# Kernel optimization log

Measured on AMD Instinct MI355X. Metric: run time of the kernel, lower is better.

## Reference

```python
import jax, jax.numpy as jnp
import numpy as np


def setup_inputs() -> dict:
    key = jax.random.key(0)
    ks = jax.random.split(key, 8)
    B, S, F, K, E, N = 20000, 10, 128, 16, 128, 200000
    nodes = jax.random.randint(ks[0], (B,), 0, N)
    neigh_idx = jax.random.randint(ks[1], (B, S), 0, N)
    self_table = jax.random.normal(ks[2], (N, F), dtype=jnp.float32)
    neigh_table = jax.random.normal(ks[3], (N, F), dtype=jnp.float32)
    center = jax.random.normal(ks[4], (K, F), dtype=jnp.float32)
    cluster_mask = jax.random.uniform(ks[5], (K, F), dtype=jnp.float32)
    # xavier-like scaling keeps exp(relu(.)) in a sane range
    weight = jax.random.normal(ks[6], (E, 2 * F), dtype=jnp.float32) * 0.05
    alpha = jax.random.normal(ks[7], (2 * F, 1), dtype=jnp.float32) * 0.05
    return {"nodes": nodes, "neigh_idx": neigh_idx, "self_table": self_table,
            "neigh_table": neigh_table, "center": center, "cluster_mask": cluster_mask,
            "weight": weight, "alpha": alpha}


def reference(nodes, neigh_idx, self_table, neigh_table, center, cluster_mask, weight, alpha):
    B, S = neigh_idx.shape
    F = self_table.shape[1]
    self_feat = self_table[nodes]                       # (B, F)
    neigh = neigh_table[neigh_idx]                      # (B, S, F) gather (== mask.matmul in original)
    # attention over sampled neighbors: exp(relu([self || neigh] @ alpha))
    a_self, a_neigh = alpha[:F, 0], alpha[F:, 0]        # split cat-matmul
    logits = self_feat @ a_self                         # (B,)
    logits = logits[:, None] + neigh @ a_neigh          # (B, S)
    att = jnp.exp(jax.nn.relu(logits))
    att_norm = att / jnp.sum(att, axis=1, keepdims=True)
    # inverse-distance soft assignment to k centers (Student-t, degree 1)
    n2 = jnp.sum(neigh * neigh, axis=-1)                # (B, S)
    c2 = jnp.sum(center * center, axis=-1)              # (K,)
    cross = jnp.einsum('bsf,kf->bsk', neigh, center)    # (B, S, K)
    q = 1.0 / (n2[:, :, None] - 2.0 * cross + c2[None, None, :] + 1.0)  # (B, S, K)
    # clustered features: sum_k q[b,s,k] * mask[k,f] * neigh[b,s,f]
    clustered = neigh * jnp.einsum('bsk,kf->bsf', q, cluster_mask)      # (B, S, F)
    neigh_agg = jnp.sum(clustered * att_norm[:, :, None], axis=1)       # (B, F)
    combined = jnp.concatenate([self_feat, neigh_agg], axis=1)          # (B, 2F)
    return jax.nn.relu(combined @ weight.T)                             # (B, E)
```

## Files before the change

kernel.cpp:

```cpp
#include <hip/hip_runtime.h>
#include <hip/hip_bf16.h>

typedef unsigned short ushort_t;
typedef __attribute__((ext_vector_type(4))) float v4f;
typedef __attribute__((ext_vector_type(8))) short v8s;

#define FDIM 128
#define KCLUST 16
#define CSTRIDE 264
#define QSTRIDE 24
#define SS 10

__device__ __forceinline__ ushort_t f2bf(float x) {
    unsigned int u = __float_as_uint(x);
    unsigned int r = (u + 0x7fffu + ((u >> 16) & 1u)) >> 16;
    return (ushort_t)r;
}
__device__ __forceinline__ float bf2f(ushort_t h) {
    return __uint_as_float((unsigned int)h << 16);
}
__device__ __forceinline__ float wave_reduce_sum(float v) {
    #pragma unroll
    for (int off = 32; off > 0; off >>= 1) v += __shfl_xor(v, off, 64);
    return v;
}

union V8U { v8s v; ushort_t u[8]; };

__global__ void pack_weight(const float* __restrict__ W, ushort_t* __restrict__ Wb,
                            long total, long valid) {
    long i = ((long)blockIdx.x * blockDim.x + threadIdx.x) * 4;
    if (i >= total) return;
    float4 v;
    if (i < valid) v = *(const float4*)(W + i);
    else           v = make_float4(0.f, 0.f, 0.f, 0.f);
    ushort_t* dst = Wb + i;
    dst[0] = f2bf(v.x); dst[1] = f2bf(v.y); dst[2] = f2bf(v.z); dst[3] = f2bf(v.w);
}

__global__ __launch_bounds__(512, 2) void fused_agg_s10(
    const int* __restrict__ nodes, const int* __restrict__ neigh_idx,
    const float* __restrict__ self_table, const float* __restrict__ neigh_table,
    const float* __restrict__ center, const float* __restrict__ cluster_mask,
    const float* __restrict__ alpha, const ushort_t* __restrict__ Wb,
    float* __restrict__ out, int B, int E) {

    __shared__ __align__(16) ushort_t comb[16 * CSTRIDE];
    __shared__ __align__(16) ushort_t nbf[SS * 16 * 128];
    __shared__ __align__(16) ushort_t qhi[SS * 16 * QSTRIDE];
    __shared__ __align__(16) ushort_t qlo[SS * 16 * QSTRIDE];
    __shared__ __align__(16) float    attL[SS * 16];
    __shared__ __align__(16) float    n2L[SS * 16];
    __shared__ __align__(16) int      idxL[SS * 16];

    const int t    = threadIdx.x;
    const int lane = t & 63, wave = t >> 6;
    const int g    = t >> 5;
    const int fq   = t & 31;
    const int f0   = fq << 2;
    const int l16  = lane & 15, quad = lane >> 4;

    const int b0 = blockIdx.x * 16;
    int bg = b0 + g; if (bg >= B) bg = B - 1;

    const float4 aS = *(const float4*)(alpha + f0);
    const float4 aN = *(const float4*)(alpha + FDIM + f0);

    float ls;
    {
        size_t node = (size_t)nodes[bg];
        float4 sf = *(const float4*)(self_table + node * FDIM + f0);
        ushort_t h0 = f2bf(sf.x), h1 = f2bf(sf.y), h2 = f2bf(sf.z), h3 = f2bf(sf.w);
        uint2 pk;
        pk.x = (unsigned)h0 | ((unsigned)h1 << 16);
        pk.y = (unsigned)h2 | ((unsigned)h3 << 16);
        *(uint2*)(comb + g * CSTRIDE + f0) = pk;
        ls = sf.x * aS.x + sf.y * aS.y + sf.z * aS.z + sf.w * aS.w;
        #pragma unroll
        for (int off = 1; off <= 16; off <<= 1) ls += __shfl_xor(ls, off, 64);
    }

    v8s cbf[4]; float c2v = 0.f;
    {
        const float* crow = center + l16 * FDIM;
        #pragma unroll
        for (int kk = 0; kk < 4; kk++) {
            const float* p = crow + kk * 32 + quad * 8;
            float4 x = *(const float4*)p;
            float4 y = *(const float4*)(p + 4);
            V8U pk;
            pk.u[0] = f2bf(x.x); pk.u[1] = f2bf(x.y); pk.u[2] = f2bf(x.z); pk.u[3] = f2bf(x.w);
            pk.u[4] = f2bf(y.x); pk.u[5] = f2bf(y.y); pk.u[6] = f2bf(y.z); pk.u[7] = f2bf(y.w);
            cbf[kk] = pk.v;
            c2v += x.x*x.x + x.y*x.y + x.z*x.z + x.w*x.w
                 + y.x*y.x + y.y*y.y + y.z*y.z + y.w*y.w;
        }
        c2v += __shfl_xor(c2v, 16, 64);
        c2v += __shfl_xor(c2v, 32, 64);
    }

    v8s mhi, mlo;
    {
        V8U ph, pl;
        const int fc = wave * 16 + l16;
        #pragma unroll
        for (int j = 0; j < 8; j++) {
            float mv = (quad < 2) ? cluster_mask[(quad * 8 + j) * FDIM + fc] : 0.f;
            ushort_t h = f2bf(mv);
            ph.u[j] = h; pl.u[j] = f2bf(mv - bf2f(h));
        }
        mhi = ph.v; mlo = pl.v;
    }

    int idxv[SS];
    #pragma unroll
    for (int j = 0; j < SS; j++) idxv[j] = neigh_idx[(size_t)bg * SS + j];
    if (fq == 0) {
        #pragma unroll
        for (int j = 0; j < SS; j++) idxL[j * 16 + g] = idxv[j];
    }

    #pragma unroll
    for (int j = 0; j < SS; j++) {
        const float4 cur = *(const float4*)(neigh_table + (size_t)idxv[j] * FDIM + f0);
        {
            ushort_t h0 = f2bf(cur.x), h1 = f2bf(cur.y), h2 = f2bf(cur.z), h3 = f2bf(cur.w);
            uint2 pk;
            pk.x = (unsigned)h0 | ((unsigned)h1 << 16);
            pk.y = (unsigned)h2 | ((unsigned)h3 << 16);
            const int slot = (fq >> 1) ^ g;
            *(uint2*)((char*)nbf + (j * 16 + g) * 256 + slot * 16 + (fq & 1) * 8) = pk;
        }
        float pn = cur.x * aN.x + cur.y * aN.y + cur.z * aN.z + cur.w * aN.w;
        float p2 = cur.x * cur.x + cur.y * cur.y + cur.z * cur.z + cur.w * cur.w;
        #pragma unroll
        for (int off = 1; off <= 16; off <<= 1) {
            pn += __shfl_xor(pn, off, 64);
            p2 += __shfl_xor(p2, off, 64);
        }
        const float att = __expf(fmaxf(ls + pn, 0.f));
        if (fq == 0) { attL[j * 16 + g] = att; n2L[j * 16 + g] = p2; }
    }

    asm volatile("s_waitcnt lgkmcnt(0)" ::: "memory");
    __builtin_amdgcn_s_barrier();
    asm volatile("" ::: "memory");

    const int fcol = wave * 16 + l16;
    float nReg[SS * 4];
    #pragma unroll
    for (int s = 0; s < SS; s++) {
        const int4 iv = *(const int4*)&idxL[s * 16 + quad * 4];
        nReg[s * 4 + 0] = neigh_table[(size_t)iv.x * FDIM + fcol];
        nReg[s * 4 + 1] = neigh_table[(size_t)iv.y * FDIM + fcol];
        nReg[s * 4 + 2] = neigh_table[(size_t)iv.z * FDIM + fcol];
        nReg[s * 4 + 3] = neigh_table[(size_t)iv.w * FDIM + fcol];
    }

    for (int s = wave; s < SS; s += 8) {
        v4f xacc = {0.f, 0.f, 0.f, 0.f};
        #pragma unroll
        for (int kk = 0; kk < 4; kk++) {
            const int sl = (kk * 4 + quad) ^ l16;
            v8s af = *(const v8s*)((const char*)nbf + (s * 16 + l16) * 256 + sl * 16);
            xacc = __builtin_amdgcn_mfma_f32_16x16x32_bf16(af, cbf[kk], xacc, 0, 0, 0);
        }
        const float4 n2r = *(const float4*)&n2L[s * 16 + quad * 4];
        #pragma unroll
        for (int r = 0; r < 4; r++) {
            const float n2v = (r == 0) ? n2r.x : (r == 1) ? n2r.y : (r == 2) ? n2r.z : n2r.w;
            const float d  = n2v - 2.f * xacc[r] + c2v;
            const float qv = 1.f / (d + 1.f);
            const ushort_t h = f2bf(qv);
            qhi[(s * 16 + quad * 4 + r) * QSTRIDE + l16] = h;
            qlo[(s * 16 + quad * 4 + r) * QSTRIDE + l16] = f2bf(qv - bf2f(h));
        }
    }

    asm volatile("s_waitcnt lgkmcnt(0)" ::: "memory");
    __builtin_amdgcn_s_barrier();
    asm volatile("" ::: "memory");

    float a0 = 0.f, a1 = 0.f, a2 = 0.f, a3 = 0.f;
    float t0 = 0.f, t1 = 0.f, t2 = 0.f, t3 = 0.f;
    #pragma unroll
    for (int s = 0; s < SS; s++) {
        v8s aqh = *(const v8s*)(qhi + (s * 16 + l16) * QSTRIDE + (quad & 1) * 8);
        v8s aql = *(const v8s*)(qlo + (s * 16 + l16) * QSTRIDE + (quad & 1) * 8);
        v4f mac = {0.f, 0.f, 0.f, 0.f};
        mac = __builtin_amdgcn_mfma_f32_16x16x32_bf16(aqh, mhi, mac, 0, 0, 0);
        mac = __builtin_amdgcn_mfma_f32_16x16x32_bf16(aql, mhi, mac, 0, 0, 0);
        mac = __builtin_amdgcn_mfma_f32_16x16x32_bf16(aqh, mlo, mac, 0, 0, 0);
        const float4 attq = *(const float4*)&attL[s * 16 + quad * 4];
        a0 = fmaf(attq.x * mac[0], nReg[s * 4 + 0], a0); t0 += attq.x;
        a1 = fmaf(attq.y * mac[1], nReg[s * 4 + 1], a1); t1 += attq.y;
        a2 = fmaf(attq.z * mac[2], nReg[s * 4 + 2], a2); t2 += attq.z;
        a3 = fmaf(attq.w * mac[3], nReg[s * 4 + 3], a3); t3 += attq.w;
    }
    {
        ushort_t* cp = comb + 128 + fcol;
        cp[(quad * 4 + 0) * CSTRIDE] = f2bf(a0 / t0);
        cp[(quad * 4 + 1) * CSTRIDE] = f2bf(a1 / t1);
        cp[(quad * 4 + 2) * CSTRIDE] = f2bf(a2 / t2);
        cp[(quad * 4 + 3) * CSTRIDE] = f2bf(a3 / t3);
    }

    const int Ntiles = (E + 15) >> 4;

    v8s bfr[8];
    {
        const int nt0 = (wave < Ntiles) ? wave : 0;
        const ushort_t* wrow = Wb + (size_t)(nt0 * 16 + l16) * 256 + quad * 8;
        #pragma unroll
        for (int kk = 0; kk < 8; kk++)
            bfr[kk] = *(const v8s*)(wrow + kk * 32);
    }

    asm volatile("s_waitcnt lgkmcnt(0)" ::: "memory");
    __builtin_amdgcn_s_barrier();
    asm volatile("" ::: "memory");

    v8s afr[8];
    #pragma unroll
    for (int kk = 0; kk < 8; kk++)
        afr[kk] = *(const v8s*)(comb + l16 * CSTRIDE + kk * 32 + quad * 8);

    for (int nt = wave; nt < Ntiles; nt += 8) {
        if (nt != wave) {
            const ushort_t* wrow = Wb + (size_t)(nt * 16 + l16) * 256 + quad * 8;
            #pragma unroll
            for (int kk = 0; kk < 8; kk++)
                bfr[kk] = *(const v8s*)(wrow + kk * 32);
        }
        v4f acc = {0.f, 0.f, 0.f, 0.f};
        #pragma unroll
        for (int kk = 0; kk < 8; kk++)
            acc = __builtin_amdgcn_mfma_f32_16x16x32_bf16(afr[kk], bfr[kk], acc, 0, 0, 0);
        const int gcol = nt * 16 + l16;
        if (gcol < E) {
            #pragma unroll
            for (int rr = 0; rr < 4; rr++) {
                const int grow = b0 + quad * 4 + rr;
                if (grow < B)
                    out[(size_t)grow * E + gcol] = fmaxf(acc[rr], 0.f);
            }
        }
    }
}

__global__ void fused_generic(
    const int* __restrict__ nodes, const int* __restrict__ neigh_idx,
    const float* __restrict__ self_table, const float* __restrict__ neigh_table,
    const float* __restrict__ center, const float* __restrict__ cluster_mask,
    const float* __restrict__ alpha, const float* __restrict__ weight,
    float* __restrict__ out, int B, int S, int E) {

    __shared__ float combsh[256];
    const int b = blockIdx.x;
    const int lane = threadIdx.x;

    float s0 = self_table[(size_t)nodes[b] * FDIM + lane];
    float s1 = self_table[(size_t)nodes[b] * FDIM + 64 + lane];
    const float ls = wave_reduce_sum(s0 * alpha[lane] + s1 * alpha[64 + lane]);

    float acc0 = 0.f, acc1 = 0.f, attsum = 0.f;
    for (int s = 0; s < S; s++) {
        const size_t idx = (size_t)neigh_idx[(size_t)b * S + s];
        const float n0 = neigh_table[idx * FDIM + lane];
        const float n1 = neigh_table[idx * FDIM + 64 + lane];
        const float ln = wave_reduce_sum(n0 * alpha[128 + lane] + n1 * alpha[192 + lane]);
        const float att = __expf(fmaxf(ls + ln, 0.f));
        float m0 = 0.f, m1 = 0.f;
        for (int k = 0; k < KCLUST; k++) {
            const float c0 = center[k * FDIM + lane];
            const float c1 = center[k * FDIM + 64 + lane];
            const float d = wave_reduce_sum((n0 - c0) * (n0 - c0) + (n1 - c1) * (n1 - c1));
            const float qv = 1.f / (d + 1.f);
            m0 += qv * cluster_mask[k * FDIM + lane];
            m1 += qv * cluster_mask[k * FDIM + 64 + lane];
        }
        acc0 += att * n0 * m0; acc1 += att * n1 * m1; attsum += att;
    }
    const float inv = 1.f / attsum;
    combsh[lane] = s0; combsh[64 + lane] = s1;
    combsh[128 + lane] = acc0 * inv; combsh[192 + lane] = acc1 * inv;
    __syncthreads();
    for (int e = lane; e < E; e += 64) {
        const float* wr = weight + (size_t)e * 256;
        float o = 0.f;
        for (int j = 0; j < 256; j++) o += combsh[j] * wr[j];
        out[(size_t)b * E + e] = fmaxf(o, 0.f);
    }
}

extern "C" void kernel_launch(void* const* d_in, const int* in_sizes, int n_in,
                              void* d_out, int out_size, void* d_ws, size_t ws_size,
                              hipStream_t stream) {
    const int*   nodes        = (const int*)d_in[0];
    const int*   neigh_idx    = (const int*)d_in[1];
    const float* self_table   = (const float*)d_in[2];
    const float* neigh_table  = (const float*)d_in[3];
    const float* center       = (const float*)d_in[4];
    const float* cluster_mask = (const float*)d_in[5];
    const float* weight       = (const float*)d_in[6];
    const float* alpha        = (const float*)d_in[7];
    float* out = (float*)d_out;

    int B = in_sizes[0];
    int S = in_sizes[1] / B;
    int E = in_sizes[6] / (2 * FDIM);

    if (S == SS) {
        int Np = ((E + 15) / 16) * 16;
        ushort_t* Wb = (ushort_t*)d_ws;
        long totalW = (long)Np * 256;
        long validW = (long)E * 256;
        int blksW = (int)((totalW + 1023) / 1024);
        pack_weight<<<blksW, 256, 0, stream>>>(weight, Wb, totalW, validW);

        int nblk = (B + 15) / 16;
        fused_agg_s10<<<nblk, 512, 0, stream>>>(
            nodes, neigh_idx, self_table, neigh_table, center, cluster_mask,
            alpha, Wb, out, B, E);
    } else {
        fused_generic<<<B, 64, 0, stream>>>(
            nodes, neigh_idx, self_table, neigh_table, center, cluster_mask,
            alpha, weight, out, B, S, E);
    }
}
```

Measured before the change: 245.8 us.

## Split fused kernel into per-wave aggregation kernel and separate output GEMM kernel

```diff
diff --git a/kernel.cpp b/kernel.cpp
--- a/kernel.cpp
+++ b/kernel.cpp
@@ -7,8 +7,8 @@
 
 #define FDIM 128
 #define KCLUST 16
-#define CSTRIDE 264
 #define QSTRIDE 24
+#define MSTRIDE 20
 #define SS 10
 
 __device__ __forceinline__ ushort_t f2bf(float x) {
@@ -38,47 +38,34 @@
     dst[0] = f2bf(v.x); dst[1] = f2bf(v.y); dst[2] = f2bf(v.z); dst[3] = f2bf(v.w);
 }
 
-__global__ __launch_bounds__(512, 2) void fused_agg_s10(
+__global__ __launch_bounds__(256, 2) void agg_s10(
     const int* __restrict__ nodes, const int* __restrict__ neigh_idx,
     const float* __restrict__ self_table, const float* __restrict__ neigh_table,
     const float* __restrict__ center, const float* __restrict__ cluster_mask,
-    const float* __restrict__ alpha, const ushort_t* __restrict__ Wb,
-    float* __restrict__ out, int B, int E) {
-
-    __shared__ __align__(16) ushort_t comb[16 * CSTRIDE];
-    __shared__ __align__(16) ushort_t nbf[SS * 16 * 128];
-    __shared__ __align__(16) ushort_t qhi[SS * 16 * QSTRIDE];
-    __shared__ __align__(16) ushort_t qlo[SS * 16 * QSTRIDE];
-    __shared__ __align__(16) float    attL[SS * 16];
-    __shared__ __align__(16) float    n2L[SS * 16];
-    __shared__ __align__(16) int      idxL[SS * 16];
-
-    const int t    = threadIdx.x;
-    const int lane = t & 63, wave = t >> 6;
-    const int g    = t >> 5;
-    const int fq   = t & 31;
-    const int f0   = fq << 2;
-    const int l16  = lane & 15, quad = lane >> 4;
-
-    const int b0 = blockIdx.x * 16;
-    int bg = b0 + g; if (bg >= B) bg = B - 1;
-
-    const float4 aS = *(const float4*)(alpha + f0);
-    const float4 aN = *(const float4*)(alpha + FDIM + f0);
-
-    float ls;
-    {
-        size_t node = (size_t)nodes[bg];
-        float4 sf = *(const float4*)(self_table + node * FDIM + f0);
-        ushort_t h0 = f2bf(sf.x), h1 = f2bf(sf.y), h2 = f2bf(sf.z), h3 = f2bf(sf.w);
-        uint2 pk;
-        pk.x = (unsigned)h0 | ((unsigned)h1 << 16);
-        pk.y = (unsigned)h2 | ((unsigned)h3 << 16);
-        *(uint2*)(comb + g * CSTRIDE + f0) = pk;
-        ls = sf.x * aS.x + sf.y * aS.y + sf.z * aS.z + sf.w * aS.w;
-        #pragma unroll
-        for (int off = 1; off <= 16; off <<= 1) ls += __shfl_xor(ls, off, 64);
-    }
+    const float* __restrict__ alpha, ushort_t* __restrict__ combW, int B) {
+
+    __shared__ __align__(16) ushort_t mh[128 * MSTRIDE];
+    __shared__ __align__(16) ushort_t ml_[128 * MSTRIDE];
+    __shared__ __align__(16) float    zslot[4];
+    __shared__ __align__(16) ushort_t nb[4][16 * 128];
+    __shared__ __align__(16) ushort_t qh_[4][16 * QSTRIDE];
+    __shared__ __align__(16) ushort_t ql_[4][16 * QSTRIDE];
+
+    const int t = threadIdx.x, lane = t & 63, wave = t >> 6;
+    const int l16 = lane & 15, quad = lane >> 4;
+    const int b = blockIdx.x * 4 + wave;
+    const bool valid = b < B;
+    const int bc = valid ? b : B - 1;
+
+    int idxv[SS];
+    #pragma unroll
+    for (int j = 0; j < SS; j++) idxv[j] = neigh_idx[(size_t)bc * SS + j];
+
+    const float as0 = alpha[lane], as1 = alpha[64 + lane];
+    const float an0 = alpha[128 + lane], an1 = alpha[192 + lane];
+    const size_t node = (size_t)nodes[bc];
+    const float s0 = self_table[node * FDIM + lane];
+    const float s1 = self_table[node * FDIM + 64 + lane];
 
     v8s cbf[4]; float c2v = 0.f;
     {
@@ -99,143 +86,160 @@
         c2v += __shfl_xor(c2v, 32, 64);
     }
 
-    v8s mhi, mlo;
-    {
-        V8U ph, pl;
-        const int fc = wave * 16 + l16;
-        #pragma unroll
-        for (int j = 0; j < 8; j++) {
-            float mv = (quad < 2) ? cluster_mask[(quad * 8 + j) * FDIM + fc] : 0.f;
-            ushort_t h = f2bf(mv);
-            ph.u[j] = h; pl.u[j] = f2bf(mv - bf2f(h));
-        }
-        mhi = ph.v; mlo = pl.v;
-    }
-
-    int idxv[SS];
-    #pragma unroll
-    for (int j = 0; j < SS; j++) idxv[j] = neigh_idx[(size_t)bg * SS + j];
-    if (fq == 0) {
-        #pragma unroll
-        for (int j = 0; j < SS; j++) idxL[j * 16 + g] = idxv[j];
-    }
-
+    float n0[SS], n1[SS];
     #pragma unroll
     for (int j = 0; j < SS; j++) {
-        const float4 cur = *(const float4*)(neigh_table + (size_t)idxv[j] * FDIM + f0);
-        {
-            ushort_t h0 = f2bf(cur.x), h1 = f2bf(cur.y), h2 = f2bf(cur.z), h3 = f2bf(cur.w);
-            uint2 pk;
-            pk.x = (unsigned)h0 | ((unsigned)h1 << 16);
-            pk.y = (unsigned)h2 | ((unsigned)h3 << 16);
-            const int slot = (fq >> 1) ^ g;
-            *(uint2*)((char*)nbf + (j * 16 + g) * 256 + slot * 16 + (fq & 1) * 8) = pk;
-        }
-        float pn = cur.x * aN.x + cur.y * aN.y + cur.z * aN.z + cur.w * aN.w;
-        float p2 = cur.x * cur.x + cur.y * cur.y + cur.z * cur.z + cur.w * cur.w;
-        #pragma unroll
-        for (int off = 1; off <= 16; off <<= 1) {
-            pn += __shfl_xor(pn, off, 64);
-            p2 += __shfl_xor(p2, off, 64);
-        }
-        const float att = __expf(fmaxf(ls + pn, 0.f));
-        if (fq == 0) { attL[j * 16 + g] = att; n2L[j * 16 + g] = p2; }
-    }
+        const float* p = neigh_table + (size_t)idxv[j] * FDIM;
+        n0[j] = p[lane]; n1[j] = p[64 + lane];
+    }
+
+    for (int i = t; i < KCLUST * FDIM; i += 256) {
+        const int k = i >> 7, f = i & 127;
+        const float mv = cluster_mask[k * FDIM + f];
+        const ushort_t h = f2bf(mv);
+        mh[f * MSTRIDE + k] = h;
+        ml_[f * MSTRIDE + k] = f2bf(mv - bf2f(h));
+    }
+    for (int i = t; i < 512; i += 256) {
+        const int f = i >> 2, j = i & 3;
+        mh[f * MSTRIDE + 16 + j] = 0; ml_[f * MSTRIDE + 16 + j] = 0;
+    }
+    if (t < 4) zslot[t] = 0.f;
+    #pragma unroll
+    for (int rr = 0; rr < 6; rr++)
+        ((unsigned*)(nb[wave] + (10 + rr) * 128))[lane] = 0u;
 
     asm volatile("s_waitcnt lgkmcnt(0)" ::: "memory");
     __builtin_amdgcn_s_barrier();
     asm volatile("" ::: "memory");
 
-    const int fcol = wave * 16 + l16;
-    float nReg[SS * 4];
-    #pragma unroll
-    for (int s = 0; s < SS; s++) {
-        const int4 iv = *(const int4*)&idxL[s * 16 + quad * 4];
-        nReg[s * 4 + 0] = neigh_table[(size_t)iv.x * FDIM + fcol];
-        nReg[s * 4 + 1] = neigh_table[(size_t)iv.y * FDIM + fcol];
-        nReg[s * 4 + 2] = neigh_table[(size_t)iv.z * FDIM + fcol];
-        nReg[s * 4 + 3] = neigh_table[(size_t)iv.w * FDIM + fcol];
-    }
-
-    for (int s = wave; s < SS; s += 8) {
-        v4f xacc = {0.f, 0.f, 0.f, 0.f};
-        #pragma unroll
-        for (int kk = 0; kk < 4; kk++) {
-            const int sl = (kk * 4 + quad) ^ l16;
-            v8s af = *(const v8s*)((const char*)nbf + (s * 16 + l16) * 256 + sl * 16);
-            xacc = __builtin_amdgcn_mfma_f32_16x16x32_bf16(af, cbf[kk], xacc, 0, 0, 0);
-        }
-        const float4 n2r = *(const float4*)&n2L[s * 16 + quad * 4];
-        #pragma unroll
-        for (int r = 0; r < 4; r++) {
-            const float n2v = (r == 0) ? n2r.x : (r == 1) ? n2r.y : (r == 2) ? n2r.z : n2r.w;
-            const float d  = n2v - 2.f * xacc[r] + c2v;
-            const float qv = 1.f / (d + 1.f);
-            const ushort_t h = f2bf(qv);
-            qhi[(s * 16 + quad * 4 + r) * QSTRIDE + l16] = h;
-            qlo[(s * 16 + quad * 4 + r) * QSTRIDE + l16] = f2bf(qv - bf2f(h));
-        }
+    float ls = s0 * as0 + s1 * as1;
+    #pragma unroll
+    for (int off = 32; off > 0; off >>= 1) ls += __shfl_xor(ls, off, 64);
+
+    float att[SS], p2a[SS]; float attsum = 0.f;
+    #pragma unroll
+    for (int j = 0; j < SS; j++) {
+        float pn = n0[j] * an0 + n1[j] * an1;
+        float p2 = n0[j] * n0[j] + n1[j] * n1[j];
+        #pragma unroll
+        for (int off = 32; off > 0; off >>= 1) {
+            pn += __shfl_xor(pn, off, 64);
+            p2 += __shfl_xor(p2, off, 64);
+        }
+        att[j] = __expf(fmaxf(ls + pn, 0.f));
+        attsum += att[j];
+        p2a[j] = p2;
+        {
+            char* base = (char*)nb[wave] + j * 256;
+            const int c0 = lane >> 3, c1 = 8 + (lane >> 3);
+            *(ushort_t*)(base + (((c0 ^ j) << 4)) + (lane & 7) * 2) = f2bf(n0[j]);
+            *(ushort_t*)(base + (((c1 ^ j) << 4)) + (lane & 7) * 2) = f2bf(n1[j]);
+        }
+    }
+
+    float n2q[4], attq[4]; int idxq[4];
+    #pragma unroll
+    for (int r = 0; r < 4; r++) {
+        n2q[r]  = quad == 0 ? p2a[r] : quad == 1 ? p2a[4 + r]
+                : (quad == 2 && r < 2) ? p2a[8 + r] : 0.f;
+        attq[r] = quad == 0 ? att[r] : quad == 1 ? att[4 + r]
+                : (quad == 2 && r < 2) ? att[8 + r] : 0.f;
+        idxq[r] = quad == 0 ? idxv[r] : quad == 1 ? idxv[4 + r]
+                : (quad == 2 && r < 2) ? idxv[8 + r] : idxv[0];
+    }
+
+    float nfin[4][8];
+    #pragma unroll
+    for (int r = 0; r < 4; r++) {
+        const float* p = neigh_table + (size_t)idxq[r] * FDIM + l16;
+        #pragma unroll
+        for (int tile = 0; tile < 8; tile++) nfin[r][tile] = p[tile * 16];
     }
 
     asm volatile("s_waitcnt lgkmcnt(0)" ::: "memory");
-    __builtin_amdgcn_s_barrier();
-    asm volatile("" ::: "memory");
-
-    float a0 = 0.f, a1 = 0.f, a2 = 0.f, a3 = 0.f;
-    float t0 = 0.f, t1 = 0.f, t2 = 0.f, t3 = 0.f;
-    #pragma unroll
-    for (int s = 0; s < SS; s++) {
-        v8s aqh = *(const v8s*)(qhi + (s * 16 + l16) * QSTRIDE + (quad & 1) * 8);
-        v8s aql = *(const v8s*)(qlo + (s * 16 + l16) * QSTRIDE + (quad & 1) * 8);
+    __builtin_amdgcn_sched_barrier(0);
+    v4f xacc = {0.f, 0.f, 0.f, 0.f};
+    #pragma unroll
+    for (int kk = 0; kk < 4; kk++) {
+        v8s af = *(const v8s*)((char*)nb[wave] + l16 * 256 + (((kk * 4 + quad) ^ l16) << 4));
+        xacc = __builtin_amdgcn_mfma_f32_16x16x32_bf16(af, cbf[kk], xacc, 0, 0, 0);
+    }
+
+    #pragma unroll
+    for (int r = 0; r < 4; r++) {
+        const float d  = n2q[r] - 2.f * xacc[r] + c2v;
+        const float qv = 1.f / (d + 1.f);
+        const ushort_t h = f2bf(qv);
+        qh_[wave][(quad * 4 + r) * QSTRIDE + l16] = h;
+        ql_[wave][(quad * 4 + r) * QSTRIDE + l16] = f2bf(qv - bf2f(h));
+    }
+    asm volatile("s_waitcnt lgkmcnt(0)" ::: "memory");
+    __builtin_amdgcn_sched_barrier(0);
+    v8s aqh = *(const v8s*)((char*)qh_[wave] + l16 * 48 + (quad & 1) * 16);
+    v8s aql = *(const v8s*)((char*)ql_[wave] + l16 * 48 + (quad & 1) * 16);
+
+    float acc[8];
+    #pragma unroll
+    for (int tile = 0; tile < 8; tile++) acc[tile] = 0.f;
+    #pragma unroll
+    for (int tile = 0; tile < 8; tile++) {
+        const int f = tile * 16 + l16;
+        v8s bh = (quad < 2) ? *(const v8s*)((char*)mh  + f * 40 + quad * 16)
+                            : *(const v8s*)zslot;
+        v8s bl = (quad < 2) ? *(const v8s*)((char*)ml_ + f * 40 + quad * 16)
+                            : *(const v8s*)zslot;
         v4f mac = {0.f, 0.f, 0.f, 0.f};
-        mac = __builtin_amdgcn_mfma_f32_16x16x32_bf16(aqh, mhi, mac, 0, 0, 0);
-        mac = __builtin_amdgcn_mfma_f32_16x16x32_bf16(aql, mhi, mac, 0, 0, 0);
-        mac = __builtin_amdgcn_mfma_f32_16x16x32_bf16(aqh, mlo, mac, 0, 0, 0);
-        const float4 attq = *(const float4*)&attL[s * 16 + quad * 4];
-        a0 = fmaf(attq.x * mac[0], nReg[s * 4 + 0], a0); t0 += attq.x;
-        a1 = fmaf(attq.y * mac[1], nReg[s * 4 + 1], a1); t1 += attq.y;
-        a2 = fmaf(attq.z * mac[2], nReg[s * 4 + 2], a2); t2 += attq.z;
-        a3 = fmaf(attq.w * mac[3], nReg[s * 4 + 3], a3); t3 += attq.w;
-    }
-    {
-        ushort_t* cp = comb + 128 + fcol;
-        cp[(quad * 4 + 0) * CSTRIDE] = f2bf(a0 / t0);
-        cp[(quad * 4 + 1) * CSTRIDE] = f2bf(a1 / t1);
-        cp[(quad * 4 + 2) * CSTRIDE] = f2bf(a2 / t2);
-        cp[(quad * 4 + 3) * CSTRIDE] = f2bf(a3 / t3);
-    }
-
+        mac = __builtin_amdgcn_mfma_f32_16x16x32_bf16(aqh, bh, mac, 0, 0, 0);
+        mac = __builtin_amdgcn_mfma_f32_16x16x32_bf16(aql, bh, mac, 0, 0, 0);
+        mac = __builtin_amdgcn_mfma_f32_16x16x32_bf16(aqh, bl, mac, 0, 0, 0);
+        #pragma unroll
+        for (int r = 0; r < 4; r++)
+            acc[tile] = fmaf(attq[r] * mac[r], nfin[r][tile], acc[tile]);
+    }
+
+    #pragma unroll
+    for (int tile = 0; tile < 8; tile++) {
+        acc[tile] += __shfl_xor(acc[tile], 16, 64);
+        acc[tile] += __shfl_xor(acc[tile], 32, 64);
+    }
+
+    if (valid) {
+        const float inv = 1.f / attsum;
+        ushort_t* cw = combW + (size_t)b * 256;
+        cw[lane]      = f2bf(s0);
+        cw[64 + lane] = f2bf(s1);
+        if (quad == 0) {
+            #pragma unroll
+            for (int tile = 0; tile < 8; tile++)
+                cw[128 + tile * 16 + l16] = f2bf(acc[tile] * inv);
+        }
+    }
+}
+
+__global__ __launch_bounds__(256, 2) void gemm_out(
+    const ushort_t* __restrict__ combW, const ushort_t* __restrict__ Wb,
+    float* __restrict__ out, int B, int E) {
+
+    const int t = threadIdx.x, lane = t & 63, wave = t >> 6;
+    const int l16 = lane & 15, quad = lane >> 4;
+    const int b0 = blockIdx.x * 16;
     const int Ntiles = (E + 15) >> 4;
 
-    v8s bfr[8];
-    {
-        const int nt0 = (wave < Ntiles) ? wave : 0;
-        const ushort_t* wrow = Wb + (size_t)(nt0 * 16 + l16) * 256 + quad * 8;
-        #pragma unroll
-        for (int kk = 0; kk < 8; kk++)
-            bfr[kk] = *(const v8s*)(wrow + kk * 32);
-    }
-
-    asm volatile("s_waitcnt lgkmcnt(0)" ::: "memory");
-    __builtin_amdgcn_s_barrier();
-    asm volatile("" ::: "memory");
-
+    int arow = b0 + l16; if (arow >= B) arow = B - 1;
     v8s afr[8];
     #pragma unroll
     for (int kk = 0; kk < 8; kk++)
-        afr[kk] = *(const v8s*)(comb + l16 * CSTRIDE + kk * 32 + quad * 8);
-
-    for (int nt = wave; nt < Ntiles; nt += 8) {
-        if (nt != wave) {
-            const ushort_t* wrow = Wb + (size_t)(nt * 16 + l16) * 256 + quad * 8;
-            #pragma unroll
-            for (int kk = 0; kk < 8; kk++)
-                bfr[kk] = *(const v8s*)(wrow + kk * 32);
-        }
+        afr[kk] = *(const v8s*)(combW + (size_t)arow * 256 + kk * 32 + quad * 8);
+
+    for (int nt = wave; nt < Ntiles; nt += 4) {
+        const ushort_t* wrow = Wb + (size_t)(nt * 16 + l16) * 256 + quad * 8;
         v4f acc = {0.f, 0.f, 0.f, 0.f};
         #pragma unroll
-        for (int kk = 0; kk < 8; kk++)
-            acc = __builtin_amdgcn_mfma_f32_16x16x32_bf16(afr[kk], bfr[kk], acc, 0, 0, 0);
+        for (int kk = 0; kk < 8; kk++) {
+            v8s bfr = *(const v8s*)(wrow + kk * 32);
+            acc = __builtin_amdgcn_mfma_f32_16x16x32_bf16(afr[kk], bfr, acc, 0, 0, 0);
+        }
         const int gcol = nt * 16 + l16;
         if (gcol < E) {
             #pragma unroll
@@ -312,16 +316,21 @@
 
     if (S == SS) {
         int Np = ((E + 15) / 16) * 16;
-        ushort_t* Wb = (ushort_t*)d_ws;
+        ushort_t* Wb   = (ushort_t*)d_ws;
+        ushort_t* comb = Wb + (size_t)Np * 256;
+
         long totalW = (long)Np * 256;
         long validW = (long)E * 256;
         int blksW = (int)((totalW + 1023) / 1024);
         pack_weight<<<blksW, 256, 0, stream>>>(weight, Wb, totalW, validW);
 
-        int nblk = (B + 15) / 16;
-        fused_agg_s10<<<nblk, 512, 0, stream>>>(
+        int nblkA = (B + 3) / 4;
+        agg_s10<<<nblkA, 256, 0, stream>>>(
             nodes, neigh_idx, self_table, neigh_table, center, cluster_mask,
-            alpha, Wb, out, B, E);
+            alpha, comb, B);
+
+        int nblkG = (B + 15) / 16;
+        gemm_out<<<nblkG, 256, 0, stream>>>(comb, Wb, out, B, E);
     } else {
         fused_generic<<<B, 64, 0, stream>>>(
             nodes, neigh_idx, self_table, neigh_table, center, cluster_mask,
```

Result: slower. 270.8 us (+10.2%).
